# Kernel tuning notes

Measured on AMD Instinct MI355X. Metric: run time of the kernel, lower is better.

Reference implementation:

```python
import jax, jax.numpy as jnp
import numpy as np

TOPK = 16          # static stand-in for dense_to_sparse(A_virtual): top-k neighbors per master node
LAMBDA_ATTN = 1.0  # VirtualGeneration temperature
GAMMA = 4.0        # gaussian radial basis width
R_CENTERS = 8      # radial_embedding.out_dim
NEG = -1e9


def _sh(v):
    # stand-in spherical harmonics: 16 monomials (lmax=3-ish) of the unit direction
    n = jnp.linalg.norm(v, axis=-1, keepdims=True)
    u = v / (n + 1e-9)
    x, y, z = u[:, 0], u[:, 1], u[:, 2]
    o = jnp.ones_like(x)
    return jnp.stack([o, x, y, z, x * x, y * y, z * z, x * y, x * z, y * z,
                      x * x * x, y * y * y, z * z * z, x * x * y, y * y * z, z * z * x], axis=-1)


def _radial(r):
    # gaussian radial basis, r: [E,1] -> [E,R]
    centers = jnp.linspace(0.0, 5.0, R_CENTERS, dtype=r.dtype)
    return jnp.exp(-GAMMA * (r - centers[None, :]) ** 2)


def _msgs(x, src, dst, sh, feats, Wr, wsh, n):
    # MACE-style conv message aggregation: radial-gated, SH-modulated gather/scatter
    gate = feats @ Wr                               # [E, Cin]
    msg = x[src] * gate * (sh @ wsh)[:, None]       # [E, Cin]
    return jax.ops.segment_sum(msg, dst, num_segments=n)


def _forward(h, pos, edge_index, edge_sh, edge_feats,
             W_loc_r, w_loc_sh, W_loc_out, W_prod_loc,
             W_ms1, b_ms1, W_ms2, b_ms2, Wq, Wk,
             W_a1, b_a1, W_a2, b_a2,
             W_h_r, w_h_sh, W_h_out, W_prod_h):
    N, D = h.shape
    D2 = W_loc_out.shape[1]
    S = W_ms1.shape[0]
    src, dst = edge_index[0], edge_index[1]

    # --- local conv + prod skip (h_local) ---
    h_up = _msgs(h, src, dst, edge_sh, edge_feats, W_loc_r, w_loc_sh, N) @ W_loc_out  # [N, D2]
    h_local = h_up @ W_prod_loc + jnp.pad(h, ((0, 0), (0, D2 - D)))
    h_scalar = h_local[:, :S]

    # --- master selection (MLP -> sigmoid -> hard threshold) ---
    m = jax.nn.sigmoid(jax.nn.relu(h_scalar @ W_ms1 + b_ms1) @ W_ms2 + b_ms2)[:, 0]
    mf = (m > 0.5).astype(h.dtype)

    # --- induced master-master edges: mask instead of dynamic subgraph extraction ---
    pair = mf[src] * mf[dst]
    vec_i = pos[src] - pos[dst]
    len_i = jnp.linalg.norm(vec_i, axis=-1, keepdims=True)
    sh_i = _sh(vec_i)
    rf_i = _radial(len_i) * pair[:, None]  # induced full_weights == 1, masked to master pairs

    # --- virtual edge generation: dense attention scores among masters, static top-k ---
    q = h_scalar @ Wq
    kk = h_scalar @ Wk
    scores_nn = (q @ kk.T) / (np.sqrt(S).astype(np.float32) * LAMBDA_ATTN)  # [N, N]
    pair_ok = (mf[:, None] * mf[None, :]) * (1.0 - jnp.eye(N, dtype=h.dtype))  # no self loops
    scores_nn = jnp.where(pair_ok > 0, scores_nn, NEG)
    topv, topi = jax.lax.top_k(scores_nn, TOPK)        # [N, K]
    vsrc = jnp.repeat(jnp.arange(N), TOPK)             # [N*K]
    vdst = topi.reshape(-1)
    vvalid = (topv.reshape(-1) > NEG / 2).astype(h.dtype)

    vec_v = pos[vsrc] - pos[vdst]
    len_v = jnp.linalg.norm(vec_v, axis=-1, keepdims=True)
    sh_v = _sh(vec_v)
    rf_v = _radial(len_v)

    # --- scatter-softmax attention over virtual edges (per destination) ---
    attn_in = jnp.concatenate([h_scalar[vsrc], h_scalar[vdst], rf_v], axis=-1)
    sc = (jax.nn.relu(attn_in @ W_a1 + b_a1) @ W_a2 + b_a2)[:, 0]
    sc = jnp.where(vvalid > 0, sc, NEG)
    mx = jax.ops.segment_max(sc, vdst, num_segments=N)
    ex = jnp.where(vvalid > 0, jnp.exp(sc - mx[vdst]), 0.0)
    den = jax.ops.segment_sum(ex, vdst, num_segments=N)
    wv = ex / (den[vdst] + 1e-12)
    rf_v = rf_v * wv[:, None]

    # --- hierarchical conv over induced + virtual master edges ---
    agg = (_msgs(h_local, src, dst, sh_i, rf_i, W_h_r, w_h_sh, N)
           + _msgs(h_local, vsrc, vdst, sh_v, rf_v, W_h_r, w_h_sh, N))
    h_m_up = agg @ W_h_out
    h_hier = (h_m_up @ W_prod_h + h_local) * mf[:, None]  # zero at non-master slots

    # --- gated combine ---
    return (1.0 - m)[:, None] * h_local + m[:, None] * h_hier


def setup_inputs():
    key = jax.random.key(0)
    ks = jax.random.split(key, 24)
    N, E, D, D2, S, R, L, HID = 4096, 131072, 128, 256, 128, 8, 16, 64

    def w(k, shape):
        return (jax.random.normal(k, shape, jnp.float32) / np.sqrt(shape[0]).astype(np.float32))

    return dict(
        h=jax.random.normal(ks[0], (N, D), jnp.float32),
        pos=jax.random.normal(ks[1], (N, 3), jnp.float32),
        edge_index=jax.random.randint(ks[2], (2, E), 0, N),
        edge_sh=jax.random.normal(ks[3], (E, L), jnp.float32),
        edge_feats=jax.random.normal(ks[4], (E, R), jnp.float32),
        batch=jnp.zeros((N,), jnp.int32),
        W_loc_r=w(ks[5], (R, D)),
        w_loc_sh=jax.random.normal(ks[6], (L,), jnp.float32) / 4.0,
        W_loc_out=w(ks[7], (D, D2)),
        W_prod_loc=w(ks[8], (D2, D2)),
        W_ms1=w(ks[9], (S, HID)), b_ms1=jnp.zeros((HID,), jnp.float32),
        W_ms2=w(ks[10], (HID, 1)), b_ms2=jnp.zeros((1,), jnp.float32),
        Wq=w(ks[11], (S, S)), Wk=w(ks[12], (S, S)),
        W_a1=w(ks[13], (2 * S + R, S)), b_a1=jnp.zeros((S,), jnp.float32),
        W_a2=w(ks[14], (S, 1)), b_a2=jnp.zeros((1,), jnp.float32),
        W_h_r=w(ks[15], (R, D2)),
        w_h_sh=jax.random.normal(ks[16], (L,), jnp.float32) / 4.0,
        W_h_out=w(ks[17], (D2, D2)),
        W_prod_h=w(ks[18], (D2, D2)),
    )


def reference(h, pos, edge_index, edge_sh, edge_feats, batch,
              W_loc_r, w_loc_sh, W_loc_out, W_prod_loc,
              W_ms1, b_ms1, W_ms2, b_ms2, Wq, Wk,
              W_a1, b_a1, W_a2, b_a2,
              W_h_r, w_h_sh, W_h_out, W_prod_h):
    # batch is unused by the original forward as well
    return _forward(h, pos, edge_index, edge_sh, edge_feats,
                    W_loc_r, w_loc_sh, W_loc_out, W_prod_loc,
                    W_ms1, b_ms1, W_ms2, b_ms2, Wq, Wk,
                    W_a1, b_a1, W_a2, b_a2,
                    W_h_r, w_h_sh, W_h_out, W_prod_h)
```

## Files before the change

kernel.cpp:

```cpp
#include <hip/hip_runtime.h>

typedef unsigned int u32;
typedef unsigned long long u64;

#define NN 4096
#define EE 131072
#define DD 128
#define D2 256
#define SS 128
#define RR 8
#define LL 16
#define HH 64
#define TK 16
#define VSTRIDE 32
#define VV2 (NN*VSTRIDE)
#define NEGF -1000000000.0f
#define MNEGF -3.0e38f
#define SCLF 11.313708305358886719f
#define DELTA 1.0e-3f
#define CHUNK 1024
#define NSLICE 8
#define CAND2 136
#define RCH 32
#define VCH 64
#define MAXCH_R 8192
#define MAXCH_V 5184

__device__ __forceinline__ float fadd(float a, float b) { return __fadd_rn(a, b); }
__device__ __forceinline__ float fsub(float a, float b) { return __fsub_rn(a, b); }
__device__ __forceinline__ float fmul(float a, float b) { return __fmul_rn(a, b); }
__device__ __forceinline__ float ffma(float a, float b, float c) { return __fmaf_rn(a, b, c); }

enum : size_t {
  B_CNTR   = 0,
  B_CNTV   = 16384,
  B_MXE    = 32768,
  ZERO_END = 49152,
  B_STARTR = 49152,
  B_STARTV = 69632,
  B_LISTR  = 90112,
  B_LISTV  = 614400,
  B_TOPI   = 1138688,
  B_WFAC   = 1662976,
  B_AMSG   = 2187264,
  B_HUP    = 4284416,
  B_HLOC   = 8478720,
  B_T1     = 12673024,
  B_MARR   = 13721600,
  B_MF     = 13737984,
  B_Q      = 13754368,
  B_KT     = 15851520,
  B_SC     = 17948672,
  B_WV     = 18472960,
  B_SUMR   = 18997248,
  B_SUMV   = 23191552,
  B_AGG    = 27385856,
  B_HMUP   = 31580160,
  B_CURR   = 35774464,
  B_CURV   = 35790848,
  B_P1     = 35807232,
  B_P2     = 37904384,
  B_TOTAL  = 40001536,
  B_ERP    = B_Q,
  B_EVP    = B_HUP,
  B_SCHUNK = B_SUMR,
  B_CANDF  = B_AMSG,
  B_CHT    = B_HUP + 3145728,
  O_CHJV   = 64,
  O_CHPV   = 64 + 4*MAXCH_V,
  O_CHJR   = 64 + 8*MAXCH_V,
  O_CHPR   = 64 + 8*MAXCH_V + 4*MAXCH_R,
  B_CHT2   = 40001536,
  B_SBIG   = 41943040,
  B_CANDB  = 109051904,
  B_WCAT   = 113508352,
  B_QKP    = 113770496,
  WS_BIG   = 122159104
};

__global__ void count_keys(const int* __restrict__ keys, int n, u32* __restrict__ cnt) {
  int e = blockIdx.x * 256 + threadIdx.x;
  if (e >= n) return;
  int d = keys[e];
  if (d >= 0) atomicAdd(&cnt[d], 1u);
}

__global__ __launch_bounds__(256) void scan_ex_par(const u32* __restrict__ cnt,
                                                   u32* __restrict__ start,
                                                   u32* __restrict__ cursor, int n,
                                                   int csz, u32* __restrict__ chCnt,
                                                   int* __restrict__ chJ,
                                                   int* __restrict__ chP) {
  __shared__ u32 part[256];
  __shared__ u32 cpart[256];
  int t = threadIdx.x;
  int per = n / 256;
  u32 s = 0;
  for (int i = 0; i < per; ++i) s += cnt[t*per + i];
  part[t] = s;
  __syncthreads();
  if (t == 0) {
    u32 run = 0;
    for (int i = 0; i < 256; ++i) { u32 v = part[i]; part[i] = run; run += v; }
    start[n] = run;
  }
  __syncthreads();
  u32 run = part[t];
  for (int i = 0; i < per; ++i) {
    int k = t*per + i;
    start[k] = run;
    cursor[k] = run;
    run += cnt[k];
  }
  if (csz > 0) {
    u32 cc = 0;
    for (int i = 0; i < per; ++i) {
      u32 len = cnt[t*per + i];
      cc += (len + (u32)csz - 1u) / (u32)csz;
    }
    cpart[t] = cc;
    __syncthreads();
    if (t == 0) {
      u32 r2 = 0;
      for (int i = 0; i < 256; ++i) { u32 v = cpart[i]; cpart[i] = r2; r2 += v; }
      *chCnt = r2;
    }
    __syncthreads();
    u32 b = cpart[t];
    u32 sb = part[t];
    for (int i = 0; i < per; ++i) {
      int k = t*per + i;
      u32 len = cnt[k];
      u32 nch = (len + (u32)csz - 1u) / (u32)csz;
      for (u32 kk = 0; kk < nch; ++kk) { chJ[b] = k; chP[b] = (int)(sb + kk*(u32)csz); ++b; }
      sb += len;
    }
  }
}

__global__ void fill_atomic(const int* __restrict__ keys, int n,
                            u32* __restrict__ cursor, int* __restrict__ list) {
  int e = blockIdx.x * 256 + threadIdx.x;
  if (e >= n) return;
  int d = keys[e];
  if (d < 0) return;
  u32 p = atomicAdd(&cursor[d], 1u);
  list[p] = e;
}

__global__ void build_chunks(const u32* __restrict__ start, int nseg, int csz,
                             u32* __restrict__ cnt, int* __restrict__ chJ,
                             int* __restrict__ chP) {
  int j = blockIdx.x * 256 + threadIdx.x;
  if (j >= nseg) return;
  u32 s0 = start[j], s1 = start[j + 1];
  if (s0 >= s1) return;
  int nch = (int)((s1 - s0) + (u32)csz - 1) / csz;
  u32 b = atomicAdd(cnt, (u32)nch);
  for (int k = 0; k < nch; ++k) {
    chJ[b + k] = j;
    chP[b + k] = (int)(s0 + (u32)k * (u32)csz);
  }
}

__global__ void concat_w(const float* __restrict__ Wq, const float* __restrict__ Wk,
                         const float* __restrict__ Wa1, float* __restrict__ Wcat) {
  int i = blockIdx.x * 256 + threadIdx.x;
  if (i >= 128*512) return;
  int k = i >> 9, c = i & 511;
  float v;
  if (c < 128)      v = Wq[k*128 + c];
  else if (c < 256) v = Wk[k*128 + (c - 128)];
  else if (c < 384) v = Wa1[(size_t)k*128 + (c - 256)];
  else              v = Wa1[(size_t)(128 + k)*128 + (c - 384)];
  Wcat[i] = v;
}

__global__ __launch_bounds__(128) void rep_msgs1(
    const float* __restrict__ h, const int* __restrict__ ei,
    const float* __restrict__ efeat, const float* __restrict__ esh,
    const float* __restrict__ wlsh,
    const float* __restrict__ Wr,
    const u32* __restrict__ startR, const int* __restrict__ listR,
    float* __restrict__ amsg)
{
  __shared__ int   ssrc[64];
  __shared__ float sshv[64];
  __shared__ float sef[64][8];
  int d = blockIdx.x, c = threadIdx.x;
  float wr[RR];
  #pragma unroll
  for (int r = 0; r < RR; ++r) wr[r] = Wr[r*DD + c];
  float acc = 0.f;
  u32 s0 = startR[d], s1 = startR[d + 1];
  for (u32 t0 = s0; t0 < s1; t0 += 64) {
    int tl = (int)(s1 - t0 < 64u ? s1 - t0 : 64u);
    if (c < tl) {
      int e = listR[t0 + c];
      ssrc[c] = ei[e];
      float s = 0.f;
      #pragma unroll
      for (int l = 0; l < LL; ++l) s = ffma(esh[(size_t)e*LL + l], wlsh[l], s);
      sshv[c] = s;
      const float4* fe = reinterpret_cast<const float4*>(&efeat[(size_t)e*RR]);
      float4 f0 = fe[0], f1 = fe[1];
      sef[c][0]=f0.x; sef[c][1]=f0.y; sef[c][2]=f0.z; sef[c][3]=f0.w;
      sef[c][4]=f1.x; sef[c][5]=f1.y; sef[c][6]=f1.z; sef[c][7]=f1.w;
    }
    __syncthreads();
    int k = 0;
    for (; k + 4 <= tl; k += 4) {
      float h0 = h[(size_t)ssrc[k  ]*DD + c];
      float h1 = h[(size_t)ssrc[k+1]*DD + c];
      float h2 = h[(size_t)ssrc[k+2]*DD + c];
      float h3 = h[(size_t)ssrc[k+3]*DD + c];
      float g0 = 0.f, g1 = 0.f, g2 = 0.f, g3 = 0.f;
      #pragma unroll
      for (int r = 0; r < RR; ++r) {
        g0 = ffma(sef[k  ][r], wr[r], g0);
        g1 = ffma(sef[k+1][r], wr[r], g1);
        g2 = ffma(sef[k+2][r], wr[r], g2);
        g3 = ffma(sef[k+3][r], wr[r], g3);
      }
      acc = fadd(acc, fmul(fmul(h0, g0), sshv[k  ]));
      acc = fadd(acc, fmul(fmul(h1, g1), sshv[k+1]));
      acc = fadd(acc, fmul(fmul(h2, g2), sshv[k+2]));
      acc = fadd(acc, fmul(fmul(h3, g3), sshv[k+3]));
    }
    for (; k < tl; ++k) {
      float hv = h[(size_t)ssrc[k]*DD + c];
      float g = 0.f;
      #pragma unroll
      for (int r = 0; r < RR; ++r) g = ffma(sef[k][r], wr[r], g);
      acc = fadd(acc, fmul(fmul(hv, g), sshv[k]));
    }
    __syncthreads();
  }
  amsg[d*DD + c] = acc;
}

__global__ __launch_bounds__(256) void gemm64(
    const float* __restrict__ A, int lda,
    const float* __restrict__ B, int ldb,
    float* __restrict__ C, int ldc,
    int K, int mode,
    const float* __restrict__ x1,
    const float* __restrict__ marr, const float* __restrict__ mfarr,
    float* __restrict__ outp)
{
  __shared__ float As[16][68];
  __shared__ float Bs[16][68];
  int tid = threadIdx.x;
  int bm = blockIdx.x << 6, bn = blockIdx.y << 6;
  int tm = ((tid >> 4) << 2), tn = ((tid & 15) << 2);
  float acc[4][4] = {};
  for (int k0 = 0; k0 < K; k0 += 16) {
    #pragma unroll
    for (int t = 0; t < 4; ++t) {
      int idx = tid + (t << 8);
      int r = idx >> 4, c = idx & 15;
      As[c][r] = A[(size_t)(bm + r)*lda + k0 + c];
      int rb = idx >> 6, cb = idx & 63;
      Bs[rb][cb] = B[(size_t)(k0 + rb)*ldb + bn + cb];
    }
    __syncthreads();
    #pragma unroll
    for (int kk = 0; kk < 16; ++kk) {
      float4 av = *reinterpret_cast<const float4*>(&As[kk][tm]);
      float4 bv = *reinterpret_cast<const float4*>(&Bs[kk][tn]);
      float a0 = av.x, a1 = av.y, a2 = av.z, a3 = av.w;
      float b0 = bv.x, b1 = bv.y, b2 = bv.z, b3 = bv.w;
      acc[0][0]=ffma(a0,b0,acc[0][0]); acc[0][1]=ffma(a0,b1,acc[0][1]);
      acc[0][2]=ffma(a0,b2,acc[0][2]); acc[0][3]=ffma(a0,b3,acc[0][3]);
      acc[1][0]=ffma(a1,b0,acc[1][0]); acc[1][1]=ffma(a1,b1,acc[1][1]);
      acc[1][2]=ffma(a1,b2,acc[1][2]); acc[1][3]=ffma(a1,b3,acc[1][3]);
      acc[2][0]=ffma(a2,b0,acc[2][0]); acc[2][1]=ffma(a2,b1,acc[2][1]);
      acc[2][2]=ffma(a2,b2,acc[2][2]); acc[2][3]=ffma(a2,b3,acc[2][3]);
      acc[3][0]=ffma(a3,b0,acc[3][0]); acc[3][1]=ffma(a3,b1,acc[3][1]);
      acc[3][2]=ffma(a3,b2,acc[3][2]); acc[3][3]=ffma(a3,b3,acc[3][3]);
    }
    __syncthreads();
  }
  #pragma unroll
  for (int ii = 0; ii < 4; ++ii) {
    int r = bm + tm + ii;
    #pragma unroll
    for (int jj = 0; jj < 4; ++jj) {
      int c = bn + tn + jj;
      float v = acc[ii][jj];
      if (mode == 0) {
        C[(size_t)r*ldc + c] = v;
      } else if (mode == 1) {
        if (c < DD) v = fadd(v, x1[(size_t)r*DD + c]);
        C[(size_t)r*ldc + c] = v;
      } else if (mode == 2) {
        float hl = x1[(size_t)r*D2 + c];
        float hh = fmul(fadd(v, hl), mfarr[r]);
        float m = marr[r];
        outp[(size_t)r*D2 + c] = fadd(fmul(fsub(1.f, m), hl), fmul(m, hh));
      } else {
        C[(size_t)c*ldc + r] = v;
      }
    }
  }
}

__global__ __launch_bounds__(256, 2) void gemm_score2b(
    const float* __restrict__ A, int lda,
    const float* __restrict__ Krm, int ldk,
    const float* __restrict__ mf, int rowoff,
    float* __restrict__ S)
{
  __shared__ float As[16][136];
  __shared__ float Bs[16][136];
  int tid = threadIdx.x;
  int bm = blockIdx.x << 7;
  int bn = blockIdx.y << 7;
  int tm = ((tid >> 4) << 2);
  int tn = ((tid & 15) << 2);
  float acc[8][8] = {};
  for (int k0 = 0; k0 < SS; k0 += 16) {
    {
      int row = tid >> 1, seg = (tid & 1) << 3;
      const float4 a0 = *reinterpret_cast<const float4*>(
          &A[(size_t)(bm + row)*lda + k0 + seg]);
      const float4 a1 = *reinterpret_cast<const float4*>(
          &A[(size_t)(bm + row)*lda + k0 + seg + 4]);
      As[seg+0][row] = a0.x; As[seg+1][row] = a0.y;
      As[seg+2][row] = a0.z; As[seg+3][row] = a0.w;
      As[seg+4][row] = a1.x; As[seg+5][row] = a1.y;
      As[seg+6][row] = a1.z; As[seg+7][row] = a1.w;
    }
    {
      int col = tid >> 1, seg = (tid & 1) << 3;
      const float4 b0 = *reinterpret_cast<const float4*>(
          &Krm[(size_t)(bn + col)*ldk + k0 + seg]);
      const float4 b1 = *reinterpret_cast<const float4*>(
          &Krm[(size_t)(bn + col)*ldk + k0 + seg + 4]);
      Bs[seg+0][col] = b0.x; Bs[seg+1][col] = b0.y;
      Bs[seg+2][col] = b0.z; Bs[seg+3][col] = b0.w;
      Bs[seg+4][col] = b1.x; Bs[seg+5][col] = b1.y;
      Bs[seg+6][col] = b1.z; Bs[seg+7][col] = b1.w;
    }
    __syncthreads();
    #pragma unroll
    for (int kk = 0; kk < 16; ++kk) {
      float4 al = *reinterpret_cast<const float4*>(&As[kk][tm]);
      float4 ah = *reinterpret_cast<const float4*>(&As[kk][tm + 64]);
      float4 bl = *reinterpret_cast<const float4*>(&Bs[kk][tn]);
      float4 bh = *reinterpret_cast<const float4*>(&Bs[kk][tn + 64]);
      float a[8] = {al.x, al.y, al.z, al.w, ah.x, ah.y, ah.z, ah.w};
      float b[8] = {bl.x, bl.y, bl.z, bl.w, bh.x, bh.y, bh.z, bh.w};
      #pragma unroll
      for (int i = 0; i < 8; ++i)
        #pragma unroll
        for (int j = 0; j < 8; ++j)
          acc[i][j] = ffma(a[i], b[j], acc[i][j]);
    }
    __syncthreads();
  }
  #pragma unroll
  for (int ii = 0; ii < 8; ++ii) {
    int r = bm + ((ii < 4) ? (tm + ii) : (tm + 64 + (ii - 4)));
    int rg = rowoff + r;
    #pragma unroll
    for (int jg = 0; jg < 2; ++jg) {
      int cb = bn + tn + (jg << 6);
      float4 ov;
      {
        float s0 = __fdiv_rn(acc[ii][4*jg+0], SCLF);
        float s1 = __fdiv_rn(acc[ii][4*jg+1], SCLF);
        float s2 = __fdiv_rn(acc[ii][4*jg+2], SCLF);
        float s3 = __fdiv_rn(acc[ii][4*jg+3], SCLF);
        ov.x = ((mf[cb+0] > 0.5f) && (cb+0 != rg)) ? s0 : NEGF;
        ov.y = ((mf[cb+1] > 0.5f) && (cb+1 != rg)) ? s1 : NEGF;
        ov.z = ((mf[cb+2] > 0.5f) && (cb+2 != rg)) ? s2 : NEGF;
        ov.w = ((mf[cb+3] > 0.5f) && (cb+3 != rg)) ? s3 : NEGF;
      }
      *reinterpret_cast<float4*>(&S[(size_t)r*NN + cb]) = ov;
    }
  }
}

__device__ __forceinline__ u64 enc_key(float v, int j) {
  u32 u = __float_as_uint(v);
  u = (u & 0x80000000u) ? ~u : (u | 0x80000000u);
  return ((u64)u << 32) | (u32)(0xFFFFFFFFu - (u32)j);
}
__device__ __forceinline__ float dec_val(u64 k) {
  u32 e = (u32)(k >> 32);
  u32 u = (e & 0x80000000u) ? (e ^ 0x80000000u) : ~e;
  return __uint_as_float(u);
}
__device__ __forceinline__ int dec_idx(u64 k) {
  return (int)(0xFFFFFFFFu - (u32)k);
}

__global__ __launch_bounds__(256) void sel_part(
    const float* __restrict__ S, const float* __restrict__ mf, int rowoff,
    u64* __restrict__ cand)
{
  int wid = threadIdx.x >> 6, lane = threadIdx.x & 63;
  int task = blockIdx.x * 4 + wid;
  int lrow = task >> 3;
  int slice = task & 7;
  if (mf[rowoff + lrow] <= 0.5f) return;
  const float* sp = S + (size_t)lrow * NN + (slice << 9);
  int jb = (slice << 9) + (lane << 2);
  float4 v0 = *reinterpret_cast<const float4*>(sp + (lane << 2));
  float4 v1 = *reinterpret_cast<const float4*>(sp + 256 + (lane << 2));
  u64 kq[8];
  kq[0] = enc_key(v0.x, jb);       kq[1] = enc_key(v0.y, jb + 1);
  kq[2] = enc_key(v0.z, jb + 2);   kq[3] = enc_key(v0.w, jb + 3);
  kq[4] = enc_key(v1.x, jb + 256); kq[5] = enc_key(v1.y, jb + 257);
  kq[6] = enc_key(v1.z, jb + 258); kq[7] = enc_key(v1.w, jb + 259);
  u64 cmx = 0;
  #pragma unroll
  for (int t = 0; t < 8; ++t) cmx = (kq[t] > cmx) ? kq[t] : cmx;
  u64* cw = cand + ((size_t)lrow * NSLICE + slice) * 17;
  for (int it = 0; it < 17; ++it) {
    u64 m = cmx;
    #pragma unroll
    for (int off = 32; off > 0; off >>= 1) {
      u64 o = __shfl_down(m, off);
      if (o > m) m = o;
    }
    u64 gmax = __shfl(m, 0);
    if (cmx == gmax) {
      u64 nm = 0;
      #pragma unroll
      for (int t = 0; t < 8; ++t) {
        kq[t] = (kq[t] == gmax) ? 0ull : kq[t];
        nm = (kq[t] > nm) ? kq[t] : nm;
      }
      cmx = nm;
    }
    if (lane == 0) cw[it] = gmax;
  }
}

__global__ __launch_bounds__(256) void sel_merge(
    const u64* __restrict__ cand, int rowoff, const float* __restrict__ mf,
    int* __restrict__ topi, float* __restrict__ wfac)
{
  int tid = threadIdx.x;
  int w = tid >> 6, lane = tid & 63;
  int lrow = blockIdx.x * 4 + w;
  int row = rowoff + lrow;
  int base = row * VSTRIDE;
  if (mf[row] <= 0.5f) {
    if (lane < VSTRIDE) { topi[base + lane] = -1; wfac[base + lane] = 0.f; }
    return;
  }
  const u64* cr = cand + (size_t)lrow * CAND2;
  u64 kq[3];
  kq[0] = cr[lane];
  kq[1] = cr[64 + lane];
  kq[2] = (lane < 8) ? cr[128 + lane] : 0ull;
  u64 cmx = 0;
  #pragma unroll
  for (int t = 0; t < 3; ++t) cmx = (kq[t] > cmx) ? kq[t] : cmx;
  float v15 = 0.f, v16 = 0.f; int i15 = -1, i16 = -1;
  for (int it = 0; it < 17; ++it) {
    u64 m = cmx;
    #pragma unroll
    for (int off = 32; off > 0; off >>= 1) {
      u64 o = __shfl_down(m, off);
      if (o > m) m = o;
    }
    u64 gmax = __shfl(m, 0);
    if (cmx == gmax) {
      u64 nm = 0;
      #pragma unroll
      for (int t = 0; t < 3; ++t) {
        kq[t] = (kq[t] == gmax) ? 0ull : kq[t];
        nm = (kq[t] > nm) ? kq[t] : nm;
      }
      cmx = nm;
    }
    if (lane == 0) {
      float fv = dec_val(gmax);
      int fi = dec_idx(gmax);
      if (it < 15) {
        bool ok = fv > 0.5f * NEGF;
        topi[base + it] = ok ? fi : -1;
        wfac[base + it] = ok ? 1.f : 0.f;
      } else if (it == 15) { v15 = fv; i15 = fi; }
      else                 { v16 = fv; i16 = fi; }
    }
  }
  if (lane == 0) {
    bool b16 = v15 > 0.5f * NEGF;
    bool b17 = v16 > 0.5f * NEGF;
    bool contested = b16 && b17 && (fsub(v15, v16) < DELTA);
    topi[base + 15] = b16 ? i15 : -1;
    wfac[base + 15] = b16 ? (contested ? 0.5f : 1.f) : 0.f;
    topi[base + 16] = contested ? i16 : -1;
    wfac[base + 16] = contested ? 0.5f : 0.f;
  }
  if (lane >= 17 && lane < VSTRIDE) { topi[base + lane] = -1; wfac[base + lane] = 0.f; }
}

__global__ __launch_bounds__(64) void rep_mask(const float* __restrict__ t1,
    const float* __restrict__ b1, const float* __restrict__ W2,
    const float* __restrict__ b2, float* __restrict__ marr, float* __restrict__ mf)
{
  __shared__ float t3[HH];
  int n = blockIdx.x, hh = threadIdx.x;
  t3[hh] = fmaxf(fadd(t1[n*HH + hh], b1[hh]), 0.f);
  __syncthreads();
  if (hh == 0) {
    float acc = 0.f;
    for (int k = 0; k < HH; ++k) acc = ffma(t3[k], W2[k], acc);
    float z = fadd(acc, b2[0]);
    float m = __fdiv_rn(1.f, fadd(1.f, expf(-z)));
    marr[n] = m;
    mf[n] = (m > 0.5f) ? 1.f : 0.f;
  }
}

__device__ __forceinline__ float centerf(int r) {
  return (float)(((double)r * 5.0) / 7.0);
}

__global__ __launch_bounds__(256) void attn_edge2(
    const float* __restrict__ P1, const float* __restrict__ P2, int ldp,
    const float* __restrict__ pos, const int* __restrict__ topi,
    const float* __restrict__ Wa1, const float* __restrict__ ba1,
    const float* __restrict__ Wa2, const float* __restrict__ ba2,
    float* __restrict__ sc, u32* __restrict__ mxe)
{
  __shared__ float wsum[4];
  __shared__ float srf[2][8];
  int tid = threadIdx.x;
  int eh = tid >> 7;
  int c = tid & 127;
  int idx = blockIdx.x * 2 + eh;
  int i = idx / 17;
  int k = idx - i * 17;
  int v = (i << 5) + k;
  int j = topi[v];
  if (c < 8 && j >= 0) {
    float vx = fsub(pos[i*3+0], pos[j*3+0]);
    float vy = fsub(pos[i*3+1], pos[j*3+1]);
    float vz = fsub(pos[i*3+2], pos[j*3+2]);
    float n2 = fadd(fadd(fmul(vx,vx), fmul(vy,vy)), fmul(vz,vz));
    float len = __fsqrt_rn(n2);
    float dr = fsub(len, centerf(c));
    srf[eh][c] = expf(fmul(-4.f, fmul(dr, dr)));
  }
  __syncthreads();
  float p = 0.f;
  if (j >= 0) {
    float t = fadd(P1[(size_t)i*ldp + c], P2[(size_t)j*ldp + c]);
    #pragma unroll
    for (int r = 0; r < RR; ++r) {
      t = ffma(srf[eh][r], Wa1[(256 + r)*SS + c], t);
    }
    t = fmaxf(fadd(t, ba1[c]), 0.f);
    p = fmul(t, Wa2[c]);
  }
  #pragma unroll
  for (int off = 32; off > 0; off >>= 1) p += __shfl_down(p, off);
  int wid = tid >> 6;
  if ((tid & 63) == 0) wsum[wid] = p;
  __syncthreads();
  if ((tid & 127) == 0 && j >= 0) {
    float acc = wsum[eh*2] + wsum[eh*2 + 1];
    float s = fadd(acc, ba2[0]);
    sc[v] = s;
    u32 u = __float_as_uint(s);
    u = (u & 0x80000000u) ? ~u : (u | 0x80000000u);
    atomicMax(&mxe[j], u);
  }
}

__global__ __launch_bounds__(64) void rep_denwv2(
    const float* __restrict__ sc, const u32* __restrict__ mxe,
    const u32* __restrict__ startV, const int* __restrict__ listV,
    const float* __restrict__ wfac, float* __restrict__ wvv)
{
  int j = blockIdx.x;
  int lane = threadIdx.x;
  u32 s0 = startV[j], s1 = startV[j + 1];
  if (s0 == s1) return;
  u32 ue = mxe[j];
  u32 b = (ue & 0x80000000u) ? (ue ^ 0x80000000u) : ~ue;
  float mx = __uint_as_float(b);
  float psum = 0.f;
  for (u32 idx = s0 + lane; idx < s1; idx += 64) {
    int v = listV[idx];
    float ex = fmul(wfac[v], expf(fsub(sc[v], mx)));
    wvv[v] = ex;
    psum += ex;
  }
  #pragma unroll
  for (int off = 32; off > 0; off >>= 1) psum += __shfl_down(psum, off);
  float den = __shfl(psum, 0);
  float dd = fadd(den, 1e-12f);
  for (u32 idx = s0 + lane; idx < s1; idx += 64) {
    int v = listV[idx];
    wvv[v] = __fdiv_rn(wvv[v], dd);
  }
}

__device__ __forceinline__ float shrep(float vx, float vy, float vz,
                                       const float* __restrict__ w) {
  float n2 = fadd(fadd(fmul(vx,vx), fmul(vy,vy)), fmul(vz,vz));
  float n = __fsqrt_rn(n2);
  float dnm = fadd(n, 1e-9f);
  float x = __fdiv_rn(vx, dnm), y = __fdiv_rn(vy, dnm), z = __fdiv_rn(vz, dnm);
  float t[16];
  t[0]=1.f; t[1]=x; t[2]=y; t[3]=z;
  t[4]=fmul(x,x); t[5]=fmul(y,y); t[6]=fmul(z,z);
  t[7]=fmul(x,y); t[8]=fmul(x,z); t[9]=fmul(y,z);
  t[10]=fmul(fmul(x,x),x); t[11]=fmul(fmul(y,y),y); t[12]=fmul(fmul(z,z),z);
  t[13]=fmul(fmul(x,x),y); t[14]=fmul(fmul(y,y),z); t[15]=fmul(fmul(z,z),x);
  float s = 0.f;
  #pragma unroll
  for (int l = 0; l < 16; ++l) s = ffma(t[l], w[l], s);
  return s;
}

__global__ void edge_pre_rv(const float* __restrict__ pos, const int* __restrict__ ei,
                            const float* __restrict__ mf, const float* __restrict__ whsh,
                            const int* __restrict__ listR, float* __restrict__ erp,
                            const int* __restrict__ topi, const float* __restrict__ wvv,
                            const u32* __restrict__ startV, const int* __restrict__ listV,
                            float* __restrict__ evp) {
  int b = blockIdx.x;
  if (b < EE/256) {
    int p = b * 256 + threadIdx.x;
    int e = listR[p];
    int src = ei[e], dst = ei[EE + e];
    float* op = erp + (size_t)p * 9;
    if (mf[src] <= 0.5f || mf[dst] <= 0.5f) {
      #pragma unroll
      for (int r = 0; r < 9; ++r) op[r] = 0.f;
      return;
    }
    float vx = fsub(pos[src*3+0], pos[dst*3+0]);
    float vy = fsub(pos[src*3+1], pos[dst*3+1]);
    float vz = fsub(pos[src*3+2], pos[dst*3+2]);
    op[0] = shrep(vx, vy, vz, whsh);
    float len = __fsqrt_rn(fadd(fadd(fmul(vx,vx), fmul(vy,vy)), fmul(vz,vz)));
    #pragma unroll
    for (int r = 0; r < RR; ++r) {
      float dr = fsub(len, centerf(r));
      op[1 + r] = expf(fmul(-4.f, fmul(dr, dr)));
    }
  } else {
    int p = (b - EE/256) * 256 + threadIdx.x;
    if (p >= (int)startV[NN]) return;
    int v = listV[p];
    int i = v >> 5;
    int j = topi[v];
    float w = wvv[v];
    float* op = evp + (size_t)p * 9;
    float vx = fsub(pos[i*3+0], pos[j*3+0]);
    float vy = fsub(pos[i*3+1], pos[j*3+1]);
    float vz = fsub(pos[i*3+2], pos[j*3+2]);
    op[0] = shrep(vx, vy, vz, whsh);
    float len = __fsqrt_rn(fadd(fadd(fmul(vx,vx), fmul(vy,vy)), fmul(vz,vz)));
    #pragma unroll
    for (int r = 0; r < RR; ++r) {
      float dr = fsub(len, centerf(r));
      op[1 + r] = fmul(expf(fmul(-4.f, fmul(dr, dr))), w);
    }
  }
}

__global__ __launch_bounds__(256) void rep_msgs2r4(
    const float* __restrict__ hloc, const int* __restrict__ ei,
    const float* __restrict__ Whr, const float* __restrict__ erp,
    const u32* __restrict__ startR, const int* __restrict__ listR,
    const u32* __restrict__ cnt, const int* __restrict__ chJ,
    const int* __restrict__ chP, float* __restrict__ sumR)
{
  __shared__ int   ssrc[RCH];
  __shared__ float sep[RCH][9];
  int b = blockIdx.x;
  if (b >= (int)(*cnt)) return;
  int d = chJ[b], c = threadIdx.x;
  u32 p0 = (u32)chP[b];
  u32 p1 = startR[d + 1];
  u32 pe = p0 + RCH; if (pe < p1) p1 = pe;
  int len = (int)(p1 - p0);
  if (c < len) ssrc[c] = ei[listR[p0 + c]];
  for (int t = c; t < len*9; t += 256) (&sep[0][0])[t] = erp[(size_t)p0*9 + t];
  __syncthreads();
  float whr[RR];
  #pragma unroll
  for (int r = 0; r < RR; ++r) whr[r] = Whr[r*D2 + c];
  float acc = 0.f;
  int k = 0;
  for (; k + 4 <= len; k += 4) {
    float h0 = hloc[(size_t)ssrc[k  ]*D2 + c];
    float h1 = hloc[(size_t)ssrc[k+1]*D2 + c];
    float h2 = hloc[(size_t)ssrc[k+2]*D2 + c];
    float h3 = hloc[(size_t)ssrc[k+3]*D2 + c];
    float g0 = 0.f, g1 = 0.f, g2 = 0.f, g3 = 0.f;
    #pragma unroll
    for (int r = 0; r < RR; ++r) {
      g0 = ffma(sep[k  ][1 + r], whr[r], g0);
      g1 = ffma(sep[k+1][1 + r], whr[r], g1);
      g2 = ffma(sep[k+2][1 + r], whr[r], g2);
      g3 = ffma(sep[k+3][1 + r], whr[r], g3);
    }
    acc = fadd(acc, fmul(fmul(h0, g0), sep[k  ][0]));
    acc = fadd(acc, fmul(fmul(h1, g1), sep[k+1][0]));
    acc = fadd(acc, fmul(fmul(h2, g2), sep[k+2][0]));
    acc = fadd(acc, fmul(fmul(h3, g3), sep[k+3][0]));
  }
  for (; k < len; ++k) {
    float hv = hloc[(size_t)ssrc[k]*D2 + c];
    float g = 0.f;
    #pragma unroll
    for (int r = 0; r < RR; ++r) g = ffma(sep[k][1 + r], whr[r], g);
    acc = fadd(acc, fmul(fmul(hv, g), sep[k][0]));
  }
  atomicAdd(&sumR[(size_t)d*D2 + c], acc);
}

__global__ __launch_bounds__(256) void rep_msgs2v4(
    const float* __restrict__ hloc, const int* __restrict__ listV,
    const float* __restrict__ Whr, const float* __restrict__ evp,
    const u32* __restrict__ startV,
    const u32* __restrict__ cnt, const int* __restrict__ chJ,
    const int* __restrict__ chP, float* __restrict__ sumR)
{
  __shared__ int   si[VCH];
  __shared__ float sep[VCH][9];
  int b = blockIdx.x;
  if (b >= (int)(*cnt)) return;
  int j = chJ[b], c = threadIdx.x;
  u32 p0 = (u32)chP[b];
  u32 p1 = startV[j + 1];
  u32 pe = p0 + VCH; if (pe < p1) p1 = pe;
  int len = (int)(p1 - p0);
  if (c < len) si[c] = listV[p0 + c] >> 5;
  for (int t = c; t < len*9; t += 256) (&sep[0][0])[t] = evp[(size_t)p0*9 + t];
  __syncthreads();
  float whr[RR];
  #pragma unroll
  for (int r = 0; r < RR; ++r) whr[r] = Whr[r*D2 + c];
  float acc = 0.f;
  int k = 0;
  for (; k + 4 <= len; k += 4) {
    float h0 = hloc[(size_t)si[k  ]*D2 + c];
    float h1 = hloc[(size_t)si[k+1]*D2 + c];
    float h2 = hloc[(size_t)si[k+2]*D2 + c];
    float h3 = hloc[(size_t)si[k+3]*D2 + c];
    float g0 = 0.f, g1 = 0.f, g2 = 0.f, g3 = 0.f;
    #pragma unroll
    for (int r = 0; r < RR; ++r) {
      g0 = ffma(sep[k  ][1 + r], whr[r], g0);
      g1 = ffma(sep[k+1][1 + r], whr[r], g1);
      g2 = ffma(sep[k+2][1 + r], whr[r], g2);
      g3 = ffma(sep[k+3][1 + r], whr[r], g3);
    }
    acc = fadd(acc, fmul(fmul(h0, g0), sep[k  ][0]));
    acc = fadd(acc, fmul(fmul(h1, g1), sep[k+1][0]));
    acc = fadd(acc, fmul(fmul(h2, g2), sep[k+2][0]));
    acc = fadd(acc, fmul(fmul(h3, g3), sep[k+3][0]));
  }
  for (; k < len; ++k) {
    float hv = hloc[(size_t)si[k]*D2 + c];
    float g = 0.f;
    #pragma unroll
    for (int r = 0; r < RR; ++r) g = ffma(sep[k][1 + r], whr[r], g);
    acc = fadd(acc, fmul(fmul(hv, g), sep[k][0]));
  }
  atomicAdd(&sumR[(size_t)j*D2 + c], acc);
}

extern "C" void kernel_launch(void* const* d_in, const int* in_sizes, int n_in,
                              void* d_out, int out_size, void* d_ws, size_t ws_size,
                              hipStream_t stream)
{
  char* wsb = (char*)d_ws;
  const float* h     = (const float*)d_in[0];
  const float* pos   = (const float*)d_in[1];
  const int*   ei    = (const int*)d_in[2];
  const float* esh   = (const float*)d_in[3];
  const float* efeat = (const float*)d_in[4];
  const float* Wlr   = (const float*)d_in[6];
  const float* wlsh  = (const float*)d_in[7];
  const float* Wlo   = (const float*)d_in[8];
  const float* Wpl   = (const float*)d_in[9];
  const float* Wms1  = (const float*)d_in[10];
  const float* bms1  = (const float*)d_in[11];
  const float* Wms2  = (const float*)d_in[12];
  const float* bms2  = (const float*)d_in[13];
  const float* Wq    = (const float*)d_in[14];
  const float* Wk    = (const float*)d_in[15];
  const float* Wa1   = (const float*)d_in[16];
  const float* ba1   = (const float*)d_in[17];
  const float* Wa2   = (const float*)d_in[18];
  const float* ba2   = (const float*)d_in[19];
  const float* Whr   = (const float*)d_in[20];
  const float* whsh  = (const float*)d_in[21];
  const float* Who   = (const float*)d_in[22];
  const float* Wph   = (const float*)d_in[23];

  u32* cntR   = (u32*)(wsb + B_CNTR);
  u32* cntV   = (u32*)(wsb + B_CNTV);
  u32* mxe    = (u32*)(wsb + B_MXE);
  u32* startR = (u32*)(wsb + B_STARTR);
  u32* startV = (u32*)(wsb + B_STARTV);
  u32* curR   = (u32*)(wsb + B_CURR);
  u32* curV   = (u32*)(wsb + B_CURV);
  int* listR  = (int*)(wsb + B_LISTR);
  int* listV  = (int*)(wsb + B_LISTV);
  int* topi   = (int*)(wsb + B_TOPI);
  float* wfac = (float*)(wsb + B_WFAC);
  float* amsg = (float*)(wsb + B_AMSG);
  float* hup  = (float*)(wsb + B_HUP);
  float* hloc = (float*)(wsb + B_HLOC);
  float* t1   = (float*)(wsb + B_T1);
  float* marr = (float*)(wsb + B_MARR);
  float* mf   = (float*)(wsb + B_MF);
  float* q    = (float*)(wsb + B_Q);
  float* krm  = (float*)(wsb + B_KT);
  float* sc   = (float*)(wsb + B_SC);
  float* wvv  = (float*)(wsb + B_WV);
  float* sumR = (float*)(wsb + B_SUMR);
  float* hmup = (float*)(wsb + B_HMUP);
  float* P1   = (float*)(wsb + B_P1);
  float* P2   = (float*)(wsb + B_P2);
  float* erp  = (float*)(wsb + B_ERP);
  float* evp  = (float*)(wsb + B_EVP);

  const bool big = ws_size >= (size_t)WS_BIG;
  char* cht = wsb + (big ? B_CHT2 : B_CHT);
  u32* chCntV = (u32*)(cht);
  u32* chCntR = (u32*)(cht + 4);
  int* chJv   = (int*)(cht + O_CHJV);
  int* chPv   = (int*)(cht + O_CHPV);
  int* chJr   = (int*)(cht + O_CHJR);
  int* chPr   = (int*)(cht + O_CHPR);
  float* Sbuf = (float*)(wsb + (big ? B_SBIG : B_SCHUNK));
  u64* cand   = (u64*)(wsb + (big ? B_CANDB : B_CANDF));
  float* Wcat = (float*)(wsb + B_WCAT);
  float* QKP  = (float*)(wsb + B_QKP);

  hipMemsetAsync(d_ws, 0, ZERO_END, stream);

  count_keys<<<EE/256, 256, 0, stream>>>(ei + EE, EE, cntR);
  if (big)
    scan_ex_par<<<1, 256, 0, stream>>>(cntR, startR, curR, NN, RCH, chCntR, chJr, chPr);
  else
    scan_ex_par<<<1, 256, 0, stream>>>(cntR, startR, curR, NN, 0, nullptr, nullptr, nullptr);
  fill_atomic<<<EE/256, 256, 0, stream>>>(ei + EE, EE, curR, listR);

  rep_msgs1<<<NN, 128, 0, stream>>>(h, ei, efeat, esh, wlsh, Wlr, startR, listR, amsg);
  gemm64<<<dim3(64,4), 256, 0, stream>>>(amsg, DD, Wlo, D2, hup, D2, DD, 0,
                                         nullptr, nullptr, nullptr, nullptr);
  gemm64<<<dim3(64,4), 256, 0, stream>>>(hup, D2, Wpl, D2, hloc, D2, D2, 1,
                                         h, nullptr, nullptr, nullptr);
  gemm64<<<dim3(64,1), 256, 0, stream>>>(hloc, D2, Wms1, HH, t1, HH, SS, 0,
                                         nullptr, nullptr, nullptr, nullptr);
  rep_mask<<<NN, 64, 0, stream>>>(t1, bms1, Wms2, bms2, marr, mf);

  if (big) {
    concat_w<<<(128*512)/256, 256, 0, stream>>>(Wq, Wk, Wa1, Wcat);
    gemm64<<<dim3(64,8), 256, 0, stream>>>(hloc, D2, Wcat, 512, QKP, 512, SS, 0,
                                           nullptr, nullptr, nullptr, nullptr);
    gemm_score2b<<<dim3(NN/128, NN/128), 256, 0, stream>>>(QKP, 512, QKP + 128, 512,
                                                           mf, 0, Sbuf);
    sel_part<<<(NN*NSLICE)/4, 256, 0, stream>>>(Sbuf, mf, 0, cand);
    sel_merge<<<NN/4, 256, 0, stream>>>(cand, 0, mf, topi, wfac);
  } else {
    gemm64<<<dim3(64,2), 256, 0, stream>>>(hloc, D2, Wq, SS, q, SS, SS, 0,
                                           nullptr, nullptr, nullptr, nullptr);
    gemm64<<<dim3(64,2), 256, 0, stream>>>(hloc, D2, Wk, SS, krm, SS, SS, 0,
                                           nullptr, nullptr, nullptr, nullptr);
    for (int c0 = 0; c0 < NN; c0 += CHUNK) {
      gemm_score2b<<<dim3(CHUNK/128, NN/128), 256, 0, stream>>>(q + (size_t)c0*SS, SS,
                                                                krm, SS, mf, c0, Sbuf);
      sel_part<<<(CHUNK*NSLICE)/4, 256, 0, stream>>>(Sbuf, mf, c0, cand);
      sel_merge<<<CHUNK/4, 256, 0, stream>>>(cand, c0, mf, topi, wfac);
    }
  }

  hipMemsetAsync(wsb + B_SUMR, 0, 4194304, stream);

  count_keys<<<VV2/256, 256, 0, stream>>>(topi, VV2, cntV);
  if (big)
    scan_ex_par<<<1, 256, 0, stream>>>(cntV, startV, curV, NN, VCH, chCntV, chJv, chPv);
  else
    scan_ex_par<<<1, 256, 0, stream>>>(cntV, startV, curV, NN, 0, nullptr, nullptr, nullptr);
  fill_atomic<<<VV2/256, 256, 0, stream>>>(topi, VV2, curV, listV);

  if (big) {
    attn_edge2<<<(NN*17)/2, 256, 0, stream>>>(QKP + 256, QKP + 384, 512, pos, topi,
                                              Wa1, ba1, Wa2, ba2, sc, mxe);
  } else {
    gemm64<<<dim3(64,2), 256, 0, stream>>>(hloc, D2, Wa1, SS, P1, SS, SS, 0,
                                           nullptr, nullptr, nullptr, nullptr);
    gemm64<<<dim3(64,2), 256, 0, stream>>>(hloc, D2, Wa1 + 128*SS, SS, P2, SS, SS, 0,
                                           nullptr, nullptr, nullptr, nullptr);
    attn_edge2<<<(NN*17)/2, 256, 0, stream>>>(P1, P2, SS, pos, topi,
                                              Wa1, ba1, Wa2, ba2, sc, mxe);
  }
  rep_denwv2<<<NN, 64, 0, stream>>>(sc, mxe, startV, listV, wfac, wvv);

  if (!big) {
    hipMemsetAsync(cht, 0, 8, stream);
    build_chunks<<<NN/256, 256, 0, stream>>>(startV, NN, VCH, chCntV, chJv, chPv);
    build_chunks<<<NN/256, 256, 0, stream>>>(startR, NN, RCH, chCntR, chJr, chPr);
  }

  edge_pre_rv<<<EE/256 + (NN*17 + 255)/256, 256, 0, stream>>>(
      pos, ei, mf, whsh, listR, erp, topi, wvv, startV, listV, evp);

  rep_msgs2r4<<<MAXCH_R, 256, 0, stream>>>(hloc, ei, Whr, erp, startR, listR,
                                           chCntR, chJr, chPr, sumR);
  rep_msgs2v4<<<MAXCH_V, 256, 0, stream>>>(hloc, listV, Whr, evp, startV,
                                           chCntV, chJv, chPv, sumR);

  gemm64<<<dim3(64,4), 256, 0, stream>>>(sumR, D2, Who, D2, hmup, D2, D2, 0,
                                         nullptr, nullptr, nullptr, nullptr);
  gemm64<<<dim3(64,4), 256, 0, stream>>>(hmup, D2, Wph, D2, nullptr, D2, D2, 2,
                                         hloc, marr, mf, (float*)d_out);
}
```

Before: 497.6 us.

## Compact master nodes before score GEMM and top-k selection

Builds a compacted list of master nodes (plus an inverse map and a count) in one block. The score GEMM and partial top-k selection then run only over master rows and columns, and blocks beyond the master count exit early. This targets the dense N×N score matrix and selection work spent on non-master entries. It adds a single-block scan kernel and a memset of the candidate buffer, and it raises the workspace requirement, which could switch off the big path if the workspace is too small.

```diff
diff --git a/kernel.cpp b/kernel.cpp
--- a/kernel.cpp
+++ b/kernel.cpp
@@ -75,7 +75,10 @@
   B_CANDB  = 109051904,
   B_WCAT   = 113508352,
   B_QKP    = 113770496,
-  WS_BIG   = 122159104
+  B_VLIST  = 122159104,
+  B_RINV   = 122175488,
+  B_NV     = 122191872,
+  WS_BIG   = 122191936
 };
 
 __global__ void count_keys(const int* __restrict__ keys, int n, u32* __restrict__ cnt) {
@@ -174,6 +177,37 @@
   else if (c < 384) v = Wa1[(size_t)k*128 + (c - 256)];
   else              v = Wa1[(size_t)(128 + k)*128 + (c - 384)];
   Wcat[i] = v;
+}
+
+__global__ __launch_bounds__(256) void build_vlist(
+    const float* __restrict__ mf, int* __restrict__ vlist,
+    int* __restrict__ rinv, u32* __restrict__ nvp)
+{
+  __shared__ u32 part[256];
+  __shared__ u32 nvs;
+  int t = threadIdx.x;
+  const int per = NN / 256;
+  u32 s = 0;
+  for (int i = 0; i < per; ++i) s += (mf[t*per + i] > 0.5f) ? 1u : 0u;
+  part[t] = s;
+  __syncthreads();
+  if (t == 0) {
+    u32 run = 0;
+    for (int i = 0; i < 256; ++i) { u32 v = part[i]; part[i] = run; run += v; }
+    nvs = run;
+    *nvp = run;
+  }
+  __syncthreads();
+  u32 nv = nvs;
+  u32 run = part[t];
+  for (int i = 0; i < per; ++i) {
+    int e = t*per + i;
+    bool val = mf[e] > 0.5f;
+    int pos = val ? (int)run : (int)(nv + (u32)e - run);
+    vlist[pos] = e;
+    rinv[e] = val ? (int)run : -1;
+    if (val) ++run;
+  }
 }
 
 __global__ __launch_bounds__(128) void rep_msgs1(
@@ -382,6 +416,87 @@
   }
 }
 
+__global__ __launch_bounds__(256, 2) void gemm_score2c(
+    const float* __restrict__ QKP,
+    const int* __restrict__ vlist, const u32* __restrict__ nvp,
+    float* __restrict__ S)
+{
+  int nv = (int)(*nvp);
+  int Rb = ((nv + 127) / 128) * 128;
+  int Cb = ((nv + 511) / 512) * 512;
+  int bm = blockIdx.x << 7;
+  int bn = blockIdx.y << 7;
+  if (bm >= Rb || bn >= Cb) return;
+  __shared__ float As[16][136];
+  __shared__ float Bs[16][136];
+  int tid = threadIdx.x;
+  int tm = ((tid >> 4) << 2);
+  int tn = ((tid & 15) << 2);
+  float acc[8][8] = {};
+  for (int k0 = 0; k0 < SS; k0 += 16) {
+    {
+      int row = tid >> 1, seg = (tid & 1) << 3;
+      int gr = vlist[bm + row];
+      const float4 a0 = *reinterpret_cast<const float4*>(
+          &QKP[(size_t)gr*512 + k0 + seg]);
+      const float4 a1 = *reinterpret_cast<const float4*>(
+          &QKP[(size_t)gr*512 + k0 + seg + 4]);
+      As[seg+0][row] = a0.x; As[seg+1][row] = a0.y;
+      As[seg+2][row] = a0.z; As[seg+3][row] = a0.w;
+      As[seg+4][row] = a1.x; As[seg+5][row] = a1.y;
+      As[seg+6][row] = a1.z; As[seg+7][row] = a1.w;
+    }
+    {
+      int col = tid >> 1, seg = (tid & 1) << 3;
+      int gc = vlist[bn + col];
+      const float4 b0 = *reinterpret_cast<const float4*>(
+          &QKP[(size_t)gc*512 + 128 + k0 + seg]);
+      const float4 b1 = *reinterpret_cast<const float4*>(
+          &QKP[(size_t)gc*512 + 128 + k0 + seg + 4]);
+      Bs[seg+0][col] = b0.x; Bs[seg+1][col] = b0.y;
+      Bs[seg+2][col] = b0.z; Bs[seg+3][col] = b0.w;
+      Bs[seg+4][col] = b1.x; Bs[seg+5][col] = b1.y;
+      Bs[seg+6][col] = b1.z; Bs[seg+7][col] = b1.w;
+    }
+    __syncthreads();
+    #pragma unroll
+    for (int kk = 0; kk < 16; ++kk) {
+      float4 al = *reinterpret_cast<const float4*>(&As[kk][tm]);
+      float4 ah = *reinterpret_cast<const float4*>(&As[kk][tm + 64]);
+      float4 bl = *reinterpret_cast<const float4*>(&Bs[kk][tn]);
+      float4 bh = *reinterpret_cast<const float4*>(&Bs[kk][tn + 64]);
+      float a[8] = {al.x, al.y, al.z, al.w, ah.x, ah.y, ah.z, ah.w};
+      float b[8] = {bl.x, bl.y, bl.z, bl.w, bh.x, bh.y, bh.z, bh.w};
+      #pragma unroll
+      for (int i = 0; i < 8; ++i)
+        #pragma unroll
+        for (int j = 0; j < 8; ++j)
+          acc[i][j] = ffma(a[i], b[j], acc[i][j]);
+    }
+    __syncthreads();
+  }
+  #pragma unroll
+  for (int ii = 0; ii < 8; ++ii) {
+    int r = bm + ((ii < 4) ? (tm + ii) : (tm + 64 + (ii - 4)));
+    #pragma unroll
+    for (int jg = 0; jg < 2; ++jg) {
+      int cb = bn + tn + (jg << 6);
+      float4 ov;
+      {
+        float s0 = __fdiv_rn(acc[ii][4*jg+0], SCLF);
+        float s1 = __fdiv_rn(acc[ii][4*jg+1], SCLF);
+        float s2 = __fdiv_rn(acc[ii][4*jg+2], SCLF);
+        float s3 = __fdiv_rn(acc[ii][4*jg+3], SCLF);
+        ov.x = ((cb+0 < nv) && (cb+0 != r)) ? s0 : NEGF;
+        ov.y = ((cb+1 < nv) && (cb+1 != r)) ? s1 : NEGF;
+        ov.z = ((cb+2 < nv) && (cb+2 != r)) ? s2 : NEGF;
+        ov.w = ((cb+3 < nv) && (cb+3 != r)) ? s3 : NEGF;
+      }
+      *reinterpret_cast<float4*>(&S[(size_t)r*NN + cb]) = ov;
+    }
+  }
+}
+
 __device__ __forceinline__ u64 enc_key(float v, int j) {
   u32 u = __float_as_uint(v);
   u = (u & 0x80000000u) ? ~u : (u | 0x80000000u);
@@ -439,8 +554,63 @@
   }
 }
 
+__global__ __launch_bounds__(256) void sel_part2(
+    const float* __restrict__ S, const int* __restrict__ vlist,
+    const u32* __restrict__ nvp, u64* __restrict__ cand)
+{
+  int nv = (int)(*nvp);
+  int wid = threadIdx.x >> 6, lane = threadIdx.x & 63;
+  int task = blockIdx.x * 4 + wid;
+  int lrow = task >> 3;
+  int slice = task & 7;
+  if (lrow >= nv) return;
+  int Cb = ((nv + 511) / 512) * 512;
+  if ((slice << 9) >= Cb) return;
+  const float* sp = S + (size_t)lrow * NN + (slice << 9);
+  int cb = (slice << 9) + (lane << 2);
+  float4 v0 = *reinterpret_cast<const float4*>(sp + (lane << 2));
+  float4 v1 = *reinterpret_cast<const float4*>(sp + 256 + (lane << 2));
+  int g0 = vlist[cb + 0];
+  int g1 = vlist[cb + 1];
+  int g2 = vlist[cb + 2];
+  int g3 = vlist[cb + 3];
+  int g4 = vlist[cb + 256];
+  int g5 = vlist[cb + 257];
+  int g6 = vlist[cb + 258];
+  int g7 = vlist[cb + 259];
+  u64 kq[8];
+  kq[0] = enc_key(v0.x, g0); kq[1] = enc_key(v0.y, g1);
+  kq[2] = enc_key(v0.z, g2); kq[3] = enc_key(v0.w, g3);
+  kq[4] = enc_key(v1.x, g4); kq[5] = enc_key(v1.y, g5);
+  kq[6] = enc_key(v1.z, g6); kq[7] = enc_key(v1.w, g7);
+  u64 cmx = 0;
+  #pragma unroll
+  for (int t = 0; t < 8; ++t) cmx = (kq[t] > cmx) ? kq[t] : cmx;
+  u64* cw = cand + ((size_t)lrow * NSLICE + slice) * 17;
+  for (int it = 0; it < 17; ++it) {
+    u64 m = cmx;
+    #pragma unroll
+    for (int off = 32; off > 0; off >>= 1) {
+      u64 o = __shfl_down(m, off);
+      if (o > m) m = o;
+    }
+    u64 gmax = __shfl(m, 0);
+    if (cmx == gmax) {
+      u64 nm = 0;
+      #pragma unroll
+      for (int t = 0; t < 8; ++t) {
+        kq[t] = (kq[t] == gmax) ? 0ull : kq[t];
+        nm = (kq[t] > nm) ? kq[t] : nm;
+      }
+      cmx = nm;
+    }
+    if (lane == 0) cw[it] = gmax;
+  }
+}
+
 __global__ __launch_bounds__(256) void sel_merge(
     const u64* __restrict__ cand, int rowoff, const float* __restrict__ mf,
+    const int* __restrict__ rinv,
     int* __restrict__ topi, float* __restrict__ wfac)
 {
   int tid = threadIdx.x;
@@ -452,7 +622,8 @@
     if (lane < VSTRIDE) { topi[base + lane] = -1; wfac[base + lane] = 0.f; }
     return;
   }
-  const u64* cr = cand + (size_t)lrow * CAND2;
+  int crow = (rinv != nullptr) ? rinv[row] : lrow;
+  const u64* cr = cand + (size_t)crow * CAND2;
   u64 kq[3];
   kq[0] = cr[lane];
   kq[1] = cr[64 + lane];
@@ -843,6 +1014,9 @@
   u64* cand   = (u64*)(wsb + (big ? B_CANDB : B_CANDF));
   float* Wcat = (float*)(wsb + B_WCAT);
   float* QKP  = (float*)(wsb + B_QKP);
+  int* vlist  = (int*)(wsb + B_VLIST);
+  int* rinv   = (int*)(wsb + B_RINV);
+  u32* nvp    = (u32*)(wsb + B_NV);
 
   hipMemsetAsync(d_ws, 0, ZERO_END, stream);
 
@@ -866,10 +1040,11 @@
     concat_w<<<(128*512)/256, 256, 0, stream>>>(Wq, Wk, Wa1, Wcat);
     gemm64<<<dim3(64,8), 256, 0, stream>>>(hloc, D2, Wcat, 512, QKP, 512, SS, 0,
                                            nullptr, nullptr, nullptr, nullptr);
-    gemm_score2b<<<dim3(NN/128, NN/128), 256, 0, stream>>>(QKP, 512, QKP + 128, 512,
-                                                           mf, 0, Sbuf);
-    sel_part<<<(NN*NSLICE)/4, 256, 0, stream>>>(Sbuf, mf, 0, cand);
-    sel_merge<<<NN/4, 256, 0, stream>>>(cand, 0, mf, topi, wfac);
+    build_vlist<<<1, 256, 0, stream>>>(mf, vlist, rinv, nvp);
+    hipMemsetAsync(cand, 0, (size_t)NN * CAND2 * 8, stream);
+    gemm_score2c<<<dim3(NN/128, NN/128), 256, 0, stream>>>(QKP, vlist, nvp, Sbuf);
+    sel_part2<<<(NN*NSLICE)/4, 256, 0, stream>>>(Sbuf, vlist, nvp, cand);
+    sel_merge<<<NN/4, 256, 0, stream>>>(cand, 0, mf, rinv, topi, wfac);
   } else {
     gemm64<<<dim3(64,2), 256, 0, stream>>>(hloc, D2, Wq, SS, q, SS, SS, 0,
                                            nullptr, nullptr, nullptr, nullptr);
@@ -879,7 +1054,7 @@
       gemm_score2b<<<dim3(CHUNK/128, NN/128), 256, 0, stream>>>(q + (size_t)c0*SS, SS,
                                                                 krm, SS, mf, c0, Sbuf);
       sel_part<<<(CHUNK*NSLICE)/4, 256, 0, stream>>>(Sbuf, mf, c0, cand);
-      sel_merge<<<CHUNK/4, 256, 0, stream>>>(cand, c0, mf, topi, wfac);
+      sel_merge<<<CHUNK/4, 256, 0, stream>>>(cand, c0, mf, nullptr, topi, wfac);
     }
   }
 
```

New measurement: 473.6 us. -4.8%, faster.
